# Kernel tuning notes

Measured on AMD Instinct MI355X. Metric: run time of the kernel, lower is better.

Reference implementation:

```python
import jax, jax.numpy as jnp
import numpy as np
from jax import lax

NPOINT = 1024
K = 32
GN_GROUPS = 32
EPS = 1e-5


def farthest_point_sample(xyz, npoint):
    # xyz: (B,N,3) -> idx (B,npoint). Deterministic start at index 0.
    B, N, _ = xyz.shape
    dist0 = jnp.full((B, N), 1e10, dtype=xyz.dtype)
    far0 = jnp.zeros((B,), dtype=jnp.int32)
    barange = jnp.arange(B)

    def step(carry, _):
        dist, far = carry
        centroid = xyz[barange, far][:, None, :]              # (B,1,3)
        d = jnp.sum((xyz - centroid) ** 2, axis=-1)           # (B,N)
        dist = jnp.minimum(dist, d)
        far_new = jnp.argmax(dist, axis=-1).astype(jnp.int32)
        return (dist, far_new), far

    _, idxs = lax.scan(step, (dist0, far0), None, length=npoint)
    return idxs.T  # (B,npoint)


def conv1x1(x, w, b):
    # x: (B,Cin,M,K), w: (Cout,Cin)
    return jnp.einsum('oc,bcmk->bomk', w, x) + b[None, :, None, None]


def group_norm(x, gamma, beta, groups):
    B, C, M, Kk = x.shape
    xg = x.reshape(B, groups, C // groups, M, Kk)
    mu = xg.mean(axis=(2, 3, 4), keepdims=True)
    var = xg.var(axis=(2, 3, 4), keepdims=True)
    xg = (xg - mu) * lax.rsqrt(var + EPS)
    x = xg.reshape(B, C, M, Kk)
    return x * gamma[None, :, None, None] + beta[None, :, None, None]


def setup_inputs() -> dict:
    key = jax.random.key(0)
    ks = jax.random.split(key, 4)
    B, N, Cin = 16, 8192, 64
    hid, out_ch, in_total = 64, 128, 3 + Cin
    return {
        'xyz': jax.random.normal(ks[0], (B, N, 3), jnp.float32),
        'feat': jax.random.normal(ks[1], (B, N, Cin), jnp.float32),
        'w1': jax.random.normal(ks[2], (hid, in_total), jnp.float32) * 0.1,
        'b1': jnp.zeros((hid,), jnp.float32),
        'g1w': jnp.ones((hid,), jnp.float32),
        'g1b': jnp.zeros((hid,), jnp.float32),
        'w2': jax.random.normal(ks[3], (out_ch, hid), jnp.float32) * 0.1,
        'b2': jnp.zeros((out_ch,), jnp.float32),
        'g2w': jnp.ones((out_ch,), jnp.float32),
        'g2b': jnp.zeros((out_ch,), jnp.float32),
    }


def reference(xyz, feat, w1, b1, g1w, g1b, w2, b2, g2w, g2b):
    B, N, _ = xyz.shape
    M = min(NPOINT, N)
    k = min(K, N)

    fps_idx = farthest_point_sample(lax.stop_gradient(xyz), M)   # (B,M) ints
    batch = jnp.arange(B)[:, None]
    centroids = xyz[batch, fps_idx]                              # (B,M,3)

    # kNN via squared distances (same ordering as cdist p=2)
    d2 = (jnp.sum(centroids ** 2, -1)[:, :, None]
          + jnp.sum(xyz ** 2, -1)[:, None, :]
          - 2.0 * jnp.einsum('bmd,bnd->bmn', centroids, xyz))    # (B,M,N)
    knn_idx = lax.top_k(-d2, k)[1]                               # (B,M,k)

    b3 = jnp.arange(B)[:, None, None]
    group_xyz = xyz[b3, knn_idx]                                 # (B,M,k,3)
    delta = group_xyz - centroids[:, :, None, :]
    gfeat = feat[b3, knn_idx]                                    # (B,M,k,Cin)
    gf = jnp.concatenate([delta, gfeat], axis=-1)                # (B,M,k,3+Cin)
    x = jnp.transpose(gf, (0, 3, 1, 2))                          # (B,C,M,k)

    x = jax.nn.relu(group_norm(conv1x1(x, w1, b1), g1w, g1b, GN_GROUPS))
    x = jax.nn.relu(group_norm(conv1x1(x, w2, b2), g2w, g2b, GN_GROUPS))
    out = jnp.max(x, axis=-1)                                    # (B,out_ch,M)
    new_feat = jnp.transpose(out, (0, 2, 1))                     # (B,M,out_ch)
    return (centroids, new_feat)
```

## Files before the change

kernel.cpp:

```cpp
#include <hip/hip_runtime.h>
#include <cstdint>

#define BB 16
#define NN 8192
#define MM 1024
#define KNN 32
#define CIN 64
#define HID 64
#define OCH 128

#define KNN_OFF   0u
#define SUM1_OFF  524288u
#define SUM2_OFF  526336u
#define W2B_OFF   536576u
#define W1B_OFF   540672u
#define Y1_OFF    543744u
#define PTS4_OFF  Y1_OFF
#define FEAT16_OFF (Y1_OFF + 16777216u)

typedef unsigned long long u64;
typedef float f32x4 __attribute__((ext_vector_type(4)));
typedef float f32x2 __attribute__((ext_vector_type(2)));
typedef short bf16x8 __attribute__((ext_vector_type(8)));

__device__ __forceinline__ unsigned short f2bf(float f) {
  union { float f; unsigned u; } v; v.f = f;
  unsigned r = v.u + 0x7FFFu + ((v.u >> 16) & 1u);
  return (unsigned short)(r >> 16);
}

__device__ __forceinline__ float bf2f(unsigned short u) {
  return __uint_as_float((unsigned)u << 16);
}

__device__ __forceinline__ u64 wave_max_u64(u64 v) {
  #define DPP_RND(ctrl, rm)                                                     \
  {                                                                             \
    int lo_ = __builtin_amdgcn_update_dpp(0, (int)(unsigned)(v & 0xFFFFFFFFull),\
                                          ctrl, rm, 0xf, true);                 \
    int hi_ = __builtin_amdgcn_update_dpp(0, (int)(unsigned)(v >> 32),          \
                                          ctrl, rm, 0xf, true);                 \
    u64 o_ = ((u64)(unsigned)hi_ << 32) | (unsigned)lo_;                        \
    v = o_ > v ? o_ : v;                                                        \
  }
  DPP_RND(0x111, 0xf)
  DPP_RND(0x112, 0xf)
  DPP_RND(0x114, 0xf)
  DPP_RND(0x118, 0xf)
  DPP_RND(0x142, 0xa)
  DPP_RND(0x143, 0xc)
  #undef DPP_RND
  return v;
}

__global__ __launch_bounds__(256) void fps_init_kernel(const float* __restrict__ xyz,
                                                       const float* __restrict__ feat,
                                                       const float* __restrict__ w1,
                                                       const float* __restrict__ w2,
                                                       float* __restrict__ ws,
                                                       float* __restrict__ cent) {
  #pragma clang fp contract(off)
  __shared__ float4 sp4[NN];
  __shared__ u64 slots[MM];
  __shared__ u64 wred[2][4];
  const int tid = threadIdx.x;

  if (blockIdx.x >= 16) {
    const int t0 = (blockIdx.x - 16) * 256 + tid;
    const int stride = 240 * 256;
    for (int t = t0; t < 12288; t += stride) ws[SUM1_OFF + t] = 0.0f;
    for (int t = t0; t < 4096; t += stride) {
      unsigned lo = f2bf(w2[2 * t]);
      unsigned hi = f2bf(w2[2 * t + 1]);
      ((unsigned*)(ws + W2B_OFF))[t] = lo | (hi << 16);
    }
    for (int t = t0; t < 6144; t += stride) {
      int n = t / 96, kk = t % 96;
      float val = 0.0f;
      if (kk < 3) val = w1[n * 67 + kk];
      else if (kk >= 4 && kk < 68) val = w1[n * 67 + kk - 1];
      ((unsigned short*)(ws + W1B_OFF))[t] = f2bf(val);
    }
    for (int t = t0; t < BB * NN; t += stride) {
      float x = xyz[(size_t)t * 3], y = xyz[(size_t)t * 3 + 1], z = xyz[(size_t)t * 3 + 2];
      ((float4*)(ws + PTS4_OFF))[t] = make_float4(x, y, z, (x * x + y * y) + z * z);
    }
    for (int t = t0; t < 4194304; t += stride) {
      float2 fv = *(const float2*)(feat + 2 * (size_t)t);
      unsigned lo = f2bf(fv.x), hi = f2bf(fv.y);
      ((unsigned*)(ws + FEAT16_OFF))[t] = lo | (hi << 16);
    }
    return;
  }

  const int b = blockIdx.x;
  const int w = tid >> 6;
  const float* xp = xyz + (size_t)b * NN * 3;
  f32x2 px[16], py[16], pz[16];
  float dist0[16], dist1[16];
  #pragma unroll
  for (int i = 0; i < 16; ++i) {
    int n0 = tid + (2 * i) * 256, n1 = tid + (2 * i + 1) * 256;
    float x0 = xp[n0 * 3], y0 = xp[n0 * 3 + 1], z0 = xp[n0 * 3 + 2];
    float x1 = xp[n1 * 3], y1 = xp[n1 * 3 + 1], z1 = xp[n1 * 3 + 2];
    px[i] = (f32x2){x0, x1}; py[i] = (f32x2){y0, y1}; pz[i] = (f32x2){z0, z1};
    sp4[n0] = make_float4(x0, y0, z0, 0.0f);
    sp4[n1] = make_float4(x1, y1, z1, 0.0f);
    dist0[i] = 1e10f; dist1[i] = 1e10f;
  }
  __syncthreads();
  int far = 0;
  for (int step = 0; step < MM; ++step) {
    float4 c4 = sp4[far];
    f32x2 cx = (f32x2){c4.x, c4.x}, cy = (f32x2){c4.y, c4.y}, cz = (f32x2){c4.z, c4.z};
    float best = -1.0f; int bi = 0;
    #pragma unroll
    for (int i = 0; i < 16; ++i) {
      f32x2 dx = px[i] - cx, dy = py[i] - cy, dz = pz[i] - cz;
      f32x2 d = (dx * dx + dy * dy) + dz * dz;
      float dm0 = fminf(dist0[i], d.x);
      float dm1 = fminf(dist1[i], d.y);
      dist0[i] = dm0; dist1[i] = dm1;
      if (dm0 > best) { best = dm0; bi = tid + (2 * i) * 256; }
      if (dm1 > best) { best = dm1; bi = tid + (2 * i + 1) * 256; }
    }
    u64 key = ((u64)__float_as_uint(best) << 32) | (unsigned)(8191 - bi);
    key = wave_max_u64(key);
    const int p = step & 1;
    if ((tid & 63) == 63) wred[p][w] = key;
    __syncthreads();
    u64 k0 = wred[p][0], k1 = wred[p][1], k2 = wred[p][2], k3 = wred[p][3];
    u64 m01 = k0 > k1 ? k0 : k1;
    u64 m23 = k2 > k3 ? k2 : k3;
    u64 bk = m01 > m23 ? m01 : m23;
    if (tid == 0) slots[step] = bk;
    far = 8191 - (int)(unsigned)(bk & 0xFFFFFFFFull);
  }
  __syncthreads();
  float* co = cent + (size_t)b * MM * 3;
  for (int s = tid; s < MM; s += 256) {
    int fs = (s == 0) ? 0 : (8191 - (int)(unsigned)(slots[s - 1] & 0xFFFFFFFFull));
    float4 c = sp4[fs];
    co[s * 3 + 0] = c.x; co[s * 3 + 1] = c.y; co[s * 3 + 2] = c.z;
  }
}

__global__ __launch_bounds__(512) void knn_conv1_kernel(const float4* __restrict__ pts4,
                                                        const float* __restrict__ xyz,
                                                        const unsigned short* __restrict__ feat16,
                                                        const float* __restrict__ cent,
                                                        const unsigned short* __restrict__ w1b,
                                                        const float* __restrict__ b1,
                                                        float* __restrict__ y1,
                                                        float* __restrict__ sums1) {
  #pragma clang fp contract(off)
  __shared__ __align__(16) char smem[65536];
  __shared__ float s1acc[64], q1acc[64];
  unsigned* blo = (unsigned*)smem;
  unsigned* bhi = (unsigned*)(smem + 32768);
  u64* marea = (u64*)smem;
  int* knn_lds = (int*)smem;
  unsigned short* gsm = (unsigned short*)(smem + 8192);
  const int tid = threadIdx.x;
  const int lane = tid & 63;
  const int w = tid >> 6;
  const int b = blockIdx.x >> 4;
  const int mc = blockIdx.x & 15;
  const int m = (mc << 6) + lane;

  if (tid < 64) { s1acc[tid] = 0.0f; q1acc[tid] = 0.0f; }

  const float* cp = cent + ((size_t)b * MM + m) * 3;
  float cx = cp[0], cy = cp[1], cz = cp[2];
  float cn2 = (cx * cx + cy * cy) + cz * cz;
  u64 key[32];
  {
    u64 initk = ((u64)(__float_as_uint(3e38f) ^ 0x80000000u) << 32) | 0xFFFFFFFFull;
    #pragma unroll
    for (int j = 0; j < 32; ++j) key[j] = initk;
  }
  float kthf = 3e38f;

  auto insert = [&](u64 cand) {
    bool cprev = false; u64 kprev = 0;
    #pragma unroll
    for (int j = 0; j < 32; ++j) {
      bool cj = cand < key[j];
      u64 cur = key[j];
      u64 nv = cj ? cand : cur;
      key[j] = cprev ? kprev : nv;
      cprev = cj; kprev = cur;
    }
    unsigned hb = (unsigned)(key[31] >> 32);
    unsigned ob = (hb & 0x80000000u) ? (hb ^ 0x80000000u) : ~hb;
    kthf = __uint_as_float(ob);
  };

  int cnt = 0;
  auto flush = [&]() {
    int mcx = cnt;
    #pragma unroll
    for (int off = 1; off < 64; off <<= 1) { int o = __shfl_xor(mcx, off); mcx = o > mcx ? o : mcx; }
    for (int i = 0; i < mcx; ++i) {
      u64 cand = ((u64)bhi[i * 512 + tid] << 32) | blo[i * 512 + tid];
      if (i < cnt && cand < key[31]) insert(cand);
    }
    cnt = 0;
  };

  const int nbase = __builtin_amdgcn_readfirstlane(w * 1024);
  const float4* pb = pts4 + (size_t)b * NN + nbase;
  for (int n0 = 0; n0 < 1024; n0 += 8) {
    #pragma unroll
    for (int j = 0; j < 8; ++j) {
      int n = n0 + j;
      float4 p = pb[n];
      float dot = fmaf(cz, p.z, fmaf(cy, p.y, cx * p.x));
      float d2 = (cn2 + p.w) - 2.0f * dot;
      if (d2 <= kthf) {
        unsigned db = __float_as_uint(d2);
        unsigned fk = db ^ (((int)db < 0) ? 0xFFFFFFFFu : 0x80000000u);
        blo[cnt * 512 + tid] = (unsigned)(nbase + n);
        bhi[cnt * 512 + tid] = fk;
        cnt++;
      }
    }
    if (__ballot(cnt >= 9)) flush();
  }
  flush();
  __syncthreads();

  auto publish = [&](int a) {
    u64* ap = marea + a * 2048;
    #pragma unroll
    for (int j = 0; j < 32; ++j) ap[j * 64 + lane] = key[j];
  };
  auto merge_from = [&](int a) {
    u64* ap = marea + a * 2048;
    for (int j = 0; j < 32; ++j) {
      u64 cand = ap[j * 64 + lane];
      if (cand < key[31]) insert(cand);
    }
  };
  if (w & 1) publish(w >> 1);
  __syncthreads();
  if (!(w & 1)) merge_from(w >> 1);
  __syncthreads();
  if (w == 2) publish(0);
  if (w == 6) publish(1);
  __syncthreads();
  if (w == 0) merge_from(0);
  if (w == 4) merge_from(1);
  __syncthreads();
  if (w == 4) publish(0);
  __syncthreads();
  if (w == 0) {
    merge_from(0);
    #pragma unroll
    for (int j = 0; j < 32; ++j)
      knn_lds[lane * 32 + j] = (int)(key[j] & 0xFFFFFFFFull);
  }
  __syncthreads();

  const int quad = lane >> 4, lr = lane & 15;
  unsigned short* gf = gsm + w * (32 * 104);

  {
    int row = lane >> 1, h = (lane & 1) * 16;
    ushort4 z4 = {0, 0, 0, 0};
    *(ushort4*)(gf + row * 104 + 64 + h + 0)  = z4;
    *(ushort4*)(gf + row * 104 + 64 + h + 4)  = z4;
    *(ushort4*)(gf + row * 104 + 64 + h + 8)  = z4;
    *(ushort4*)(gf + row * 104 + 64 + h + 12) = z4;
  }
  bf16x8 bw[4][3];
  float b1v[4];
  #pragma unroll
  for (int nt = 0; nt < 4; ++nt) {
    #pragma unroll
    for (int ks = 0; ks < 3; ++ks)
      bw[nt][ks] = *(const bf16x8*)(w1b + (size_t)(nt * 16 + lr) * 96 + ks * 32 + quad * 8);
    b1v[nt] = b1[nt * 16 + lr];
  }
  float s_nt[4] = {0.f, 0.f, 0.f, 0.f};
  float q_nt[4] = {0.f, 0.f, 0.f, 0.f};
  const unsigned short* fb = feat16 + (size_t)b * NN * 64;

  for (int r = 0; r < 8; ++r) {
    const int lm = w * 8 + r;
    const int wid = b * 1024 + (mc << 6) + lm;
    int idxv = 0;
    if (lane < 32) idxv = knn_lds[lm * 32 + lane];
    __builtin_amdgcn_s_waitcnt(0);
    __builtin_amdgcn_wave_barrier();
    const float* cq = cent + (size_t)wid * 3;
    float ccx = cq[0], ccy = cq[1], ccz = cq[2];
    if (lane < 32) {
      const float* pp = xyz + ((size_t)b * NN + idxv) * 3;
      ushort4 dv;
      dv.x = f2bf(pp[0] - ccx); dv.y = f2bf(pp[1] - ccy); dv.z = f2bf(pp[2] - ccz);
      dv.w = 0;
      *(ushort4*)(gf + lane * 104) = dv;
    }
    #pragma unroll
    for (int i = 0; i < 4; ++i) {
      int v = i * 64 + lane;
      int row = v >> 3, part = v & 7;
      int ridx = __shfl(idxv, row);
      uint4 fv = *(const uint4*)(fb + (size_t)ridx * 64 + part * 8);
      *(uint2*)(gf + row * 104 + 4 + part * 8)     = make_uint2(fv.x, fv.y);
      *(uint2*)(gf + row * 104 + 4 + part * 8 + 4) = make_uint2(fv.z, fv.w);
    }
    __builtin_amdgcn_s_waitcnt(0);
    __builtin_amdgcn_wave_barrier();

    f32x4 acc[2][4];
    #pragma unroll
    for (int mt = 0; mt < 2; ++mt)
      #pragma unroll
      for (int nt = 0; nt < 4; ++nt)
        acc[mt][nt] = (f32x4){0.f, 0.f, 0.f, 0.f};
    #pragma unroll
    for (int ks = 0; ks < 3; ++ks) {
      bf16x8 a0 = *(const bf16x8*)(gf + (0 + lr) * 104 + ks * 32 + quad * 8);
      bf16x8 a1 = *(const bf16x8*)(gf + (16 + lr) * 104 + ks * 32 + quad * 8);
      #pragma unroll
      for (int nt = 0; nt < 4; ++nt) {
        acc[0][nt] = __builtin_amdgcn_mfma_f32_16x16x32_bf16(a0, bw[nt][ks], acc[0][nt], 0, 0, 0);
        acc[1][nt] = __builtin_amdgcn_mfma_f32_16x16x32_bf16(a1, bw[nt][ks], acc[1][nt], 0, 0, 0);
      }
    }
    unsigned short* yo16 = (unsigned short*)(y1 + (size_t)wid * 1024);
    #pragma unroll
    for (int mt = 0; mt < 2; ++mt)
      #pragma unroll
      for (int rg = 0; rg < 4; ++rg) {
        int row = mt * 16 + quad * 4 + rg;
        #pragma unroll
        for (int nt = 0; nt < 4; ++nt) {
          float z = acc[mt][nt][rg] + b1v[nt];
          yo16[row * 64 + nt * 16 + lr] = f2bf(z);
          s_nt[nt] += z;
          q_nt[nt] = fmaf(z, z, q_nt[nt]);
        }
      }
  }
  #pragma unroll
  for (int nt = 0; nt < 4; ++nt) {
    float s = s_nt[nt], q = q_nt[nt];
    s += __shfl_xor(s, 16); s += __shfl_xor(s, 32);
    q += __shfl_xor(q, 16); q += __shfl_xor(q, 32);
    if (quad == 0) {
      atomicAdd(&s1acc[nt * 16 + lr], s);
      atomicAdd(&q1acc[nt * 16 + lr], q);
    }
  }
  __syncthreads();
  if (tid < 64) {
    atomicAdd(&sums1[b * 128 + tid], s1acc[tid]);
    atomicAdd(&sums1[b * 128 + 64 + tid], q1acc[tid]);
  }
}

struct Conv2Frag {
  bf16x8 bfr[8][2];
  float  b2v[8];
};

__device__ __forceinline__ void load_w2_frags(const unsigned short* __restrict__ w2b,
                                              const float* __restrict__ b2,
                                              int lane, Conv2Frag& F) {
  const int quad = lane >> 4, lr = lane & 15;
  #pragma unroll
  for (int nt = 0; nt < 8; ++nt) {
    #pragma unroll
    for (int t = 0; t < 2; ++t)
      F.bfr[nt][t] = *(const bf16x8*)(w2b + (size_t)(nt * 16 + lr) * 64 + t * 32 + quad * 8);
    F.b2v[nt] = b2[nt * 16 + lr];
  }
}

__device__ __forceinline__ void conv2_wave_mfma(const float* __restrict__ y1,
                                                const float* a1s,
                                                const float* d1s,
                                                unsigned short* __restrict__ hrow,
                                                int wid, int lane,
                                                const Conv2Frag& F,
                                                f32x4 acc[2][8]) {
  const int quad = lane >> 4, lr = lane & 15;
  const int r = lane >> 1, c0 = (lane & 1) * 32;
  const unsigned short* yrow16 =
      (const unsigned short*)(y1 + (size_t)wid * 1024) + r * 64 + c0;
  const float4* ap = (const float4*)(a1s + c0);
  const float4* dp = (const float4*)(d1s + c0);
  #pragma unroll
  for (int gg = 0; gg < 4; ++gg) {
    bf16x8 yv = *(const bf16x8*)(yrow16 + gg * 8);
    float4 av0 = ap[gg * 2],     dv0 = dp[gg * 2];
    float4 av1 = ap[gg * 2 + 1], dv1 = dp[gg * 2 + 1];
    ushort4 s0, s1;
    s0.x = f2bf(fmaxf(0.0f, fmaf(bf2f((unsigned short)yv[0]), av0.x, dv0.x)));
    s0.y = f2bf(fmaxf(0.0f, fmaf(bf2f((unsigned short)yv[1]), av0.y, dv0.y)));
    s0.z = f2bf(fmaxf(0.0f, fmaf(bf2f((unsigned short)yv[2]), av0.z, dv0.z)));
    s0.w = f2bf(fmaxf(0.0f, fmaf(bf2f((unsigned short)yv[3]), av0.w, dv0.w)));
    s1.x = f2bf(fmaxf(0.0f, fmaf(bf2f((unsigned short)yv[4]), av1.x, dv1.x)));
    s1.y = f2bf(fmaxf(0.0f, fmaf(bf2f((unsigned short)yv[5]), av1.y, dv1.y)));
    s1.z = f2bf(fmaxf(0.0f, fmaf(bf2f((unsigned short)yv[6]), av1.z, dv1.z)));
    s1.w = f2bf(fmaxf(0.0f, fmaf(bf2f((unsigned short)yv[7]), av1.w, dv1.w)));
    *(ushort4*)(hrow + r * 72 + c0 + 8 * gg)     = s0;
    *(ushort4*)(hrow + r * 72 + c0 + 8 * gg + 4) = s1;
  }
  __builtin_amdgcn_s_waitcnt(0);
  __builtin_amdgcn_wave_barrier();
  #pragma unroll
  for (int mt = 0; mt < 2; ++mt)
    #pragma unroll
    for (int nt = 0; nt < 8; ++nt)
      acc[mt][nt] = (f32x4){0.f, 0.f, 0.f, 0.f};
  #pragma unroll
  for (int t = 0; t < 2; ++t) {
    bf16x8 a0 = *(const bf16x8*)(hrow + (0 + lr) * 72 + t * 32 + quad * 8);
    bf16x8 a1f = *(const bf16x8*)(hrow + (16 + lr) * 72 + t * 32 + quad * 8);
    #pragma unroll
    for (int nt = 0; nt < 8; ++nt) {
      acc[0][nt] = __builtin_amdgcn_mfma_f32_16x16x32_bf16(a0,  F.bfr[nt][t], acc[0][nt], 0, 0, 0);
      acc[1][nt] = __builtin_amdgcn_mfma_f32_16x16x32_bf16(a1f, F.bfr[nt][t], acc[1][nt], 0, 0, 0);
    }
  }
}

__global__ __launch_bounds__(256) void conv2_stats_kernel(float* __restrict__ y1,
                                                          const float* __restrict__ sums1,
                                                          const float* __restrict__ g1w,
                                                          const float* __restrict__ g1b,
                                                          const unsigned short* __restrict__ w2b,
                                                          const float* __restrict__ b2,
                                                          float* __restrict__ sums2) {
  __shared__ __align__(16) unsigned short hsm[4][32 * 72];
  __shared__ float sacc[128], qacc[128];
  __shared__ float a1s[64], d1s[64];
  const int tid = threadIdx.x, lane = tid & 63, w = tid >> 6;
  const int wid = blockIdx.x * 4 + w;
  const int b = blockIdx.x >> 8;
  if (tid < 128) { sacc[tid] = 0.0f; qacc[tid] = 0.0f; }
  if (tid < 64) {
    int c = tid, g = c >> 1;
    float S = sums1[b * 128 + g * 2] + sums1[b * 128 + g * 2 + 1];
    float Q = sums1[b * 128 + 64 + g * 2] + sums1[b * 128 + 64 + g * 2 + 1];
    float mu = S * (1.0f / 65536.0f);
    float var = Q * (1.0f / 65536.0f) - mu * mu;
    float rs = 1.0f / sqrtf(var + 1e-5f);
    float ga = g1w[c];
    a1s[c] = rs * ga;
    d1s[c] = g1b[c] - mu * rs * ga;
  }
  __syncthreads();
  Conv2Frag F;
  load_w2_frags(w2b, b2, lane, F);
  f32x4 acc[2][8];
  conv2_wave_mfma(y1, a1s, d1s, hsm[w], wid, lane, F, acc);
  const int lr = lane & 15;
  float zmx[8], zmn[8];
  #pragma unroll
  for (int nt = 0; nt < 8; ++nt) {
    float s = 0, q = 0, mx = -3e38f, mn = 3e38f;
    #pragma unroll
    for (int mt = 0; mt < 2; ++mt)
      #pragma unroll
      for (int rg = 0; rg < 4; ++rg) {
        float z = acc[mt][nt][rg] + F.b2v[nt];
        s += z; q = fmaf(z, z, q);
        mx = fmaxf(mx, z); mn = fminf(mn, z);
      }
    atomicAdd(&sacc[nt * 16 + lr], s);
    atomicAdd(&qacc[nt * 16 + lr], q);
    mx = fmaxf(mx, __shfl_xor(mx, 16)); mx = fmaxf(mx, __shfl_xor(mx, 32));
    mn = fminf(mn, __shfl_xor(mn, 16)); mn = fminf(mn, __shfl_xor(mn, 32));
    zmx[nt] = mx; zmn[nt] = mn;
  }
  if (lane < 16) {
    float* zp = y1 + (size_t)wid * 1024;
    #pragma unroll
    for (int nt = 0; nt < 8; ++nt) {
      zp[nt * 16 + lr] = zmx[nt];
      zp[128 + nt * 16 + lr] = zmn[nt];
    }
  }
  __syncthreads();
  if (tid < 128) {
    atomicAdd(&sums2[b * 256 + tid], sacc[tid]);
    atomicAdd(&sums2[b * 256 + 128 + tid], qacc[tid]);
  }
}

__global__ __launch_bounds__(256) void final_lite(const float* __restrict__ y1,
                                                  const float* __restrict__ sums2,
                                                  const float* __restrict__ g2w,
                                                  const float* __restrict__ g2b,
                                                  float* __restrict__ nf) {
  __shared__ float a2s[128], d2s[128];
  const int tid = threadIdx.x;
  const int wid0 = blockIdx.x * 2;
  const int b = wid0 >> 10;
  if (tid < 128) {
    int c = tid, g = c >> 2;
    float S = ((sums2[b * 256 + g * 4] + sums2[b * 256 + g * 4 + 1])
               + sums2[b * 256 + g * 4 + 2]) + sums2[b * 256 + g * 4 + 3];
    float Q = ((sums2[b * 256 + 128 + g * 4] + sums2[b * 256 + 128 + g * 4 + 1])
               + sums2[b * 256 + 128 + g * 4 + 2]) + sums2[b * 256 + 128 + g * 4 + 3];
    float mu = S * (1.0f / 131072.0f);
    float var = Q * (1.0f / 131072.0f) - mu * mu;
    float rs = 1.0f / sqrtf(var + 1e-5f);
    float ga = g2w[c];
    a2s[c] = rs * ga;
    d2s[c] = g2b[c] - mu * rs * ga;
  }
  __syncthreads();
  int wid = wid0 + (tid >> 7), c = tid & 127;
  const float* zp = y1 + (size_t)wid * 1024;
  float zmx = zp[c];
  float zmn = zp[128 + c];
  float az = a2s[c], dz = d2s[c];
  float z = (az >= 0.0f) ? zmx : zmn;
  nf[(size_t)wid * 128 + c] = fmaxf(0.0f, fmaf(z, az, dz));
}

extern "C" void kernel_launch(void* const* d_in, const int* in_sizes, int n_in,
                              void* d_out, int out_size, void* d_ws, size_t ws_size,
                              hipStream_t stream) {
  const float* xyz  = (const float*)d_in[0];
  const float* feat = (const float*)d_in[1];
  const float* w1   = (const float*)d_in[2];
  const float* b1   = (const float*)d_in[3];
  const float* g1w  = (const float*)d_in[4];
  const float* g1b  = (const float*)d_in[5];
  const float* w2   = (const float*)d_in[6];
  const float* b2   = (const float*)d_in[7];
  const float* g2w  = (const float*)d_in[8];
  const float* g2b  = (const float*)d_in[9];
  float* ws = (float*)d_ws;
  float* cent = (float*)d_out;
  float* nf   = (float*)d_out + BB * MM * 3;
  const float4* pts4 = (const float4*)(ws + PTS4_OFF);
  float* sums1 = ws + SUM1_OFF;
  float* sums2 = ws + SUM2_OFF;
  const unsigned short* w2b = (const unsigned short*)(ws + W2B_OFF);
  const unsigned short* w1b = (const unsigned short*)(ws + W1B_OFF);
  const unsigned short* feat16 = (const unsigned short*)(ws + FEAT16_OFF);
  float* y1 = ws + Y1_OFF;

  hipLaunchKernelGGL(fps_init_kernel, dim3(256), dim3(256), 0, stream,
                     xyz, feat, w1, w2, ws, cent);
  hipLaunchKernelGGL(knn_conv1_kernel, dim3(256), dim3(512), 0, stream,
                     pts4, xyz, feat16, cent, w1b, b1, y1, sums1);
  hipLaunchKernelGGL(conv2_stats_kernel, dim3(4096), dim3(256), 0, stream,
                     y1, sums1, g1w, g1b, w2b, b2, sums2);
  hipLaunchKernelGGL(final_lite, dim3(8192), dim3(256), 0, stream,
                     y1, sums2, g2w, g2b, nf);
}
```

Measured before the change: 1.403 ms.

## Fuse kNN/conv1, conv2 stats and final epilogue into one kernel with per-batch barriers

The kNN+conv1, conv2+GroupNorm-stats and final normalize/max kernels are merged into one kernel launched with 256 blocks. Blocks of the same batch synchronize through global atomic counters with spin-waiting, so each GroupNorm's statistics are complete before the next stage reads them. Each wave now loops over 8 rows of conv2 and accumulates statistics in registers before a single shared-atomic reduction. This removes two kernel launches and their inter-kernel gaps. In exchange it relies on all blocks of a batch being resident at once, on the counters being zeroed beforehand, and it runs conv2 with far fewer waves than the old 4096-block launch.

```diff
diff --git a/kernel.cpp b/kernel.cpp
--- a/kernel.cpp
+++ b/kernel.cpp
@@ -9,9 +9,9 @@
 #define HID 64
 #define OCH 128
 
-#define KNN_OFF   0u
 #define SUM1_OFF  524288u
 #define SUM2_OFF  526336u
+#define CNT_OFF   530432u
 #define W2B_OFF   536576u
 #define W1B_OFF   540672u
 #define Y1_OFF    543744u
@@ -145,17 +145,96 @@
   }
 }
 
-__global__ __launch_bounds__(512) void knn_conv1_kernel(const float4* __restrict__ pts4,
-                                                        const float* __restrict__ xyz,
-                                                        const unsigned short* __restrict__ feat16,
-                                                        const float* __restrict__ cent,
-                                                        const unsigned short* __restrict__ w1b,
-                                                        const float* __restrict__ b1,
-                                                        float* __restrict__ y1,
-                                                        float* __restrict__ sums1) {
+struct Conv2Frag {
+  bf16x8 bfr[8][2];
+  float  b2v[8];
+};
+
+__device__ __forceinline__ void load_w2_frags(const unsigned short* __restrict__ w2b,
+                                              const float* __restrict__ b2,
+                                              int lane, Conv2Frag& F) {
+  const int quad = lane >> 4, lr = lane & 15;
+  #pragma unroll
+  for (int nt = 0; nt < 8; ++nt) {
+    #pragma unroll
+    for (int t = 0; t < 2; ++t)
+      F.bfr[nt][t] = *(const bf16x8*)(w2b + (size_t)(nt * 16 + lr) * 64 + t * 32 + quad * 8);
+    F.b2v[nt] = b2[nt * 16 + lr];
+  }
+}
+
+__device__ __forceinline__ void conv2_wave_mfma(const float* __restrict__ y1,
+                                                const float* a1s,
+                                                const float* d1s,
+                                                unsigned short* __restrict__ hrow,
+                                                int wid, int lane,
+                                                const Conv2Frag& F,
+                                                f32x4 acc[2][8]) {
+  const int quad = lane >> 4, lr = lane & 15;
+  const int r = lane >> 1, c0 = (lane & 1) * 32;
+  const unsigned short* yrow16 =
+      (const unsigned short*)(y1 + (size_t)wid * 1024) + r * 64 + c0;
+  const float4* ap = (const float4*)(a1s + c0);
+  const float4* dp = (const float4*)(d1s + c0);
+  #pragma unroll
+  for (int gg = 0; gg < 4; ++gg) {
+    bf16x8 yv = *(const bf16x8*)(yrow16 + gg * 8);
+    float4 av0 = ap[gg * 2],     dv0 = dp[gg * 2];
+    float4 av1 = ap[gg * 2 + 1], dv1 = dp[gg * 2 + 1];
+    ushort4 s0, s1;
+    s0.x = f2bf(fmaxf(0.0f, fmaf(bf2f((unsigned short)yv[0]), av0.x, dv0.x)));
+    s0.y = f2bf(fmaxf(0.0f, fmaf(bf2f((unsigned short)yv[1]), av0.y, dv0.y)));
+    s0.z = f2bf(fmaxf(0.0f, fmaf(bf2f((unsigned short)yv[2]), av0.z, dv0.z)));
+    s0.w = f2bf(fmaxf(0.0f, fmaf(bf2f((unsigned short)yv[3]), av0.w, dv0.w)));
+    s1.x = f2bf(fmaxf(0.0f, fmaf(bf2f((unsigned short)yv[4]), av1.x, dv1.x)));
+    s1.y = f2bf(fmaxf(0.0f, fmaf(bf2f((unsigned short)yv[5]), av1.y, dv1.y)));
+    s1.z = f2bf(fmaxf(0.0f, fmaf(bf2f((unsigned short)yv[6]), av1.z, dv1.z)));
+    s1.w = f2bf(fmaxf(0.0f, fmaf(bf2f((unsigned short)yv[7]), av1.w, dv1.w)));
+    *(ushort4*)(hrow + r * 72 + c0 + 8 * gg)     = s0;
+    *(ushort4*)(hrow + r * 72 + c0 + 8 * gg + 4) = s1;
+  }
+  __builtin_amdgcn_s_waitcnt(0);
+  __builtin_amdgcn_wave_barrier();
+  #pragma unroll
+  for (int mt = 0; mt < 2; ++mt)
+    #pragma unroll
+    for (int nt = 0; nt < 8; ++nt)
+      acc[mt][nt] = (f32x4){0.f, 0.f, 0.f, 0.f};
+  #pragma unroll
+  for (int t = 0; t < 2; ++t) {
+    bf16x8 a0 = *(const bf16x8*)(hrow + (0 + lr) * 72 + t * 32 + quad * 8);
+    bf16x8 a1f = *(const bf16x8*)(hrow + (16 + lr) * 72 + t * 32 + quad * 8);
+    #pragma unroll
+    for (int nt = 0; nt < 8; ++nt) {
+      acc[0][nt] = __builtin_amdgcn_mfma_f32_16x16x32_bf16(a0,  F.bfr[nt][t], acc[0][nt], 0, 0, 0);
+      acc[1][nt] = __builtin_amdgcn_mfma_f32_16x16x32_bf16(a1f, F.bfr[nt][t], acc[1][nt], 0, 0, 0);
+    }
+  }
+}
+
+__global__ __launch_bounds__(512) void mega_kernel(const float4* __restrict__ pts4,
+                                                   const float* __restrict__ xyz,
+                                                   const unsigned short* __restrict__ feat16,
+                                                   const float* __restrict__ cent,
+                                                   const unsigned short* __restrict__ w1b,
+                                                   const float* __restrict__ b1,
+                                                   const unsigned short* __restrict__ w2b,
+                                                   const float* __restrict__ b2,
+                                                   const float* __restrict__ g1w,
+                                                   const float* __restrict__ g1b,
+                                                   const float* __restrict__ g2w,
+                                                   const float* __restrict__ g2b,
+                                                   float* __restrict__ y1,
+                                                   float* __restrict__ sums1,
+                                                   float* __restrict__ sums2,
+                                                   int* __restrict__ cnt,
+                                                   float* __restrict__ nf) {
   #pragma clang fp contract(off)
   __shared__ __align__(16) char smem[65536];
   __shared__ float s1acc[64], q1acc[64];
+  __shared__ float sacc[128], qacc[128];
+  __shared__ float a1s[64], d1s[64];
+  __shared__ float a2s[128], d2s[128];
   unsigned* blo = (unsigned*)smem;
   unsigned* bhi = (unsigned*)(smem + 32768);
   u64* marea = (u64*)smem;
@@ -169,6 +248,7 @@
   const int m = (mc << 6) + lane;
 
   if (tid < 64) { s1acc[tid] = 0.0f; q1acc[tid] = 0.0f; }
+  if (tid < 128) { sacc[tid] = 0.0f; qacc[tid] = 0.0f; }
 
   const float* cp = cent + ((size_t)b * MM + m) * 3;
   float cx = cp[0], cy = cp[1], cz = cp[2];
@@ -196,16 +276,16 @@
     kthf = __uint_as_float(ob);
   };
 
-  int cnt = 0;
+  int cntl = 0;
   auto flush = [&]() {
-    int mcx = cnt;
+    int mcx = cntl;
     #pragma unroll
     for (int off = 1; off < 64; off <<= 1) { int o = __shfl_xor(mcx, off); mcx = o > mcx ? o : mcx; }
     for (int i = 0; i < mcx; ++i) {
       u64 cand = ((u64)bhi[i * 512 + tid] << 32) | blo[i * 512 + tid];
-      if (i < cnt && cand < key[31]) insert(cand);
-    }
-    cnt = 0;
+      if (i < cntl && cand < key[31]) insert(cand);
+    }
+    cntl = 0;
   };
 
   const int nbase = __builtin_amdgcn_readfirstlane(w * 1024);
@@ -220,12 +300,12 @@
       if (d2 <= kthf) {
         unsigned db = __float_as_uint(d2);
         unsigned fk = db ^ (((int)db < 0) ? 0xFFFFFFFFu : 0x80000000u);
-        blo[cnt * 512 + tid] = (unsigned)(nbase + n);
-        bhi[cnt * 512 + tid] = fk;
-        cnt++;
+        blo[cntl * 512 + tid] = (unsigned)(nbase + n);
+        bhi[cntl * 512 + tid] = fk;
+        cntl++;
       }
     }
-    if (__ballot(cnt >= 9)) flush();
+    if (__ballot(cntl >= 9)) flush();
   }
   flush();
   __syncthreads();
@@ -360,93 +440,24 @@
     atomicAdd(&sums1[b * 128 + tid], s1acc[tid]);
     atomicAdd(&sums1[b * 128 + 64 + tid], q1acc[tid]);
   }
-}
-
-struct Conv2Frag {
-  bf16x8 bfr[8][2];
-  float  b2v[8];
-};
-
-__device__ __forceinline__ void load_w2_frags(const unsigned short* __restrict__ w2b,
-                                              const float* __restrict__ b2,
-                                              int lane, Conv2Frag& F) {
-  const int quad = lane >> 4, lr = lane & 15;
-  #pragma unroll
-  for (int nt = 0; nt < 8; ++nt) {
-    #pragma unroll
-    for (int t = 0; t < 2; ++t)
-      F.bfr[nt][t] = *(const bf16x8*)(w2b + (size_t)(nt * 16 + lr) * 64 + t * 32 + quad * 8);
-    F.b2v[nt] = b2[nt * 16 + lr];
-  }
-}
-
-__device__ __forceinline__ void conv2_wave_mfma(const float* __restrict__ y1,
-                                                const float* a1s,
-                                                const float* d1s,
-                                                unsigned short* __restrict__ hrow,
-                                                int wid, int lane,
-                                                const Conv2Frag& F,
-                                                f32x4 acc[2][8]) {
-  const int quad = lane >> 4, lr = lane & 15;
-  const int r = lane >> 1, c0 = (lane & 1) * 32;
-  const unsigned short* yrow16 =
-      (const unsigned short*)(y1 + (size_t)wid * 1024) + r * 64 + c0;
-  const float4* ap = (const float4*)(a1s + c0);
-  const float4* dp = (const float4*)(d1s + c0);
-  #pragma unroll
-  for (int gg = 0; gg < 4; ++gg) {
-    bf16x8 yv = *(const bf16x8*)(yrow16 + gg * 8);
-    float4 av0 = ap[gg * 2],     dv0 = dp[gg * 2];
-    float4 av1 = ap[gg * 2 + 1], dv1 = dp[gg * 2 + 1];
-    ushort4 s0, s1;
-    s0.x = f2bf(fmaxf(0.0f, fmaf(bf2f((unsigned short)yv[0]), av0.x, dv0.x)));
-    s0.y = f2bf(fmaxf(0.0f, fmaf(bf2f((unsigned short)yv[1]), av0.y, dv0.y)));
-    s0.z = f2bf(fmaxf(0.0f, fmaf(bf2f((unsigned short)yv[2]), av0.z, dv0.z)));
-    s0.w = f2bf(fmaxf(0.0f, fmaf(bf2f((unsigned short)yv[3]), av0.w, dv0.w)));
-    s1.x = f2bf(fmaxf(0.0f, fmaf(bf2f((unsigned short)yv[4]), av1.x, dv1.x)));
-    s1.y = f2bf(fmaxf(0.0f, fmaf(bf2f((unsigned short)yv[5]), av1.y, dv1.y)));
-    s1.z = f2bf(fmaxf(0.0f, fmaf(bf2f((unsigned short)yv[6]), av1.z, dv1.z)));
-    s1.w = f2bf(fmaxf(0.0f, fmaf(bf2f((unsigned short)yv[7]), av1.w, dv1.w)));
-    *(ushort4*)(hrow + r * 72 + c0 + 8 * gg)     = s0;
-    *(ushort4*)(hrow + r * 72 + c0 + 8 * gg + 4) = s1;
-  }
-  __builtin_amdgcn_s_waitcnt(0);
-  __builtin_amdgcn_wave_barrier();
-  #pragma unroll
-  for (int mt = 0; mt < 2; ++mt)
-    #pragma unroll
-    for (int nt = 0; nt < 8; ++nt)
-      acc[mt][nt] = (f32x4){0.f, 0.f, 0.f, 0.f};
-  #pragma unroll
-  for (int t = 0; t < 2; ++t) {
-    bf16x8 a0 = *(const bf16x8*)(hrow + (0 + lr) * 72 + t * 32 + quad * 8);
-    bf16x8 a1f = *(const bf16x8*)(hrow + (16 + lr) * 72 + t * 32 + quad * 8);
-    #pragma unroll
-    for (int nt = 0; nt < 8; ++nt) {
-      acc[0][nt] = __builtin_amdgcn_mfma_f32_16x16x32_bf16(a0,  F.bfr[nt][t], acc[0][nt], 0, 0, 0);
-      acc[1][nt] = __builtin_amdgcn_mfma_f32_16x16x32_bf16(a1f, F.bfr[nt][t], acc[1][nt], 0, 0, 0);
-    }
-  }
-}
-
-__global__ __launch_bounds__(256) void conv2_stats_kernel(float* __restrict__ y1,
-                                                          const float* __restrict__ sums1,
-                                                          const float* __restrict__ g1w,
-                                                          const float* __restrict__ g1b,
-                                                          const unsigned short* __restrict__ w2b,
-                                                          const float* __restrict__ b2,
-                                                          float* __restrict__ sums2) {
-  __shared__ __align__(16) unsigned short hsm[4][32 * 72];
-  __shared__ float sacc[128], qacc[128];
-  __shared__ float a1s[64], d1s[64];
-  const int tid = threadIdx.x, lane = tid & 63, w = tid >> 6;
-  const int wid = blockIdx.x * 4 + w;
-  const int b = blockIdx.x >> 8;
-  if (tid < 128) { sacc[tid] = 0.0f; qacc[tid] = 0.0f; }
+  __syncthreads();
+
+  if (tid == 0) {
+    __threadfence();
+    __hip_atomic_fetch_add(&cnt[b], 1, __ATOMIC_RELEASE, __HIP_MEMORY_SCOPE_AGENT);
+    for (long it = 0; it < (1L << 30); ++it) {
+      if (__hip_atomic_load(&cnt[b], __ATOMIC_ACQUIRE, __HIP_MEMORY_SCOPE_AGENT) >= 16) break;
+      __builtin_amdgcn_s_sleep(2);
+    }
+  }
+  __syncthreads();
+
   if (tid < 64) {
     int c = tid, g = c >> 1;
-    float S = sums1[b * 128 + g * 2] + sums1[b * 128 + g * 2 + 1];
-    float Q = sums1[b * 128 + 64 + g * 2] + sums1[b * 128 + 64 + g * 2 + 1];
+    float S = __hip_atomic_load(&sums1[b * 128 + g * 2], __ATOMIC_RELAXED, __HIP_MEMORY_SCOPE_AGENT)
+            + __hip_atomic_load(&sums1[b * 128 + g * 2 + 1], __ATOMIC_RELAXED, __HIP_MEMORY_SCOPE_AGENT);
+    float Q = __hip_atomic_load(&sums1[b * 128 + 64 + g * 2], __ATOMIC_RELAXED, __HIP_MEMORY_SCOPE_AGENT)
+            + __hip_atomic_load(&sums1[b * 128 + 64 + g * 2 + 1], __ATOMIC_RELAXED, __HIP_MEMORY_SCOPE_AGENT);
     float mu = S * (1.0f / 65536.0f);
     float var = Q * (1.0f / 65536.0f) - mu * mu;
     float rs = 1.0f / sqrtf(var + 1e-5f);
@@ -455,35 +466,52 @@
     d1s[c] = g1b[c] - mu * rs * ga;
   }
   __syncthreads();
+
+  unsigned short* hrow = (unsigned short*)smem + w * 2304;
   Conv2Frag F;
   load_w2_frags(w2b, b2, lane, F);
-  f32x4 acc[2][8];
-  conv2_wave_mfma(y1, a1s, d1s, hsm[w], wid, lane, F, acc);
-  const int lr = lane & 15;
-  float zmx[8], zmn[8];
+  float s2_nt[8] = {0, 0, 0, 0, 0, 0, 0, 0};
+  float q2_nt[8] = {0, 0, 0, 0, 0, 0, 0, 0};
+  for (int r = 0; r < 8; ++r) {
+    const int wid = b * 1024 + (mc << 6) + w * 8 + r;
+    f32x4 acc[2][8];
+    conv2_wave_mfma(y1, a1s, d1s, hrow, wid, lane, F, acc);
+    float zmx[8], zmn[8];
+    #pragma unroll
+    for (int nt = 0; nt < 8; ++nt) {
+      float s = 0, q = 0, mx = -3e38f, mn = 3e38f;
+      #pragma unroll
+      for (int mt = 0; mt < 2; ++mt)
+        #pragma unroll
+        for (int rg = 0; rg < 4; ++rg) {
+          float z = acc[mt][nt][rg] + F.b2v[nt];
+          s += z; q = fmaf(z, z, q);
+          mx = fmaxf(mx, z); mn = fminf(mn, z);
+        }
+      s2_nt[nt] += s; q2_nt[nt] += q;
+      mx = fmaxf(mx, __shfl_xor(mx, 16)); mx = fmaxf(mx, __shfl_xor(mx, 32));
+      mn = fminf(mn, __shfl_xor(mn, 16)); mn = fminf(mn, __shfl_xor(mn, 32));
+      zmx[nt] = mx; zmn[nt] = mn;
+    }
+    if (lane < 16) {
+      float* zp = y1 + (size_t)wid * 1024;
+      #pragma unroll
+      for (int nt = 0; nt < 8; ++nt) {
+        zp[nt * 16 + lr] = zmx[nt];
+        zp[128 + nt * 16 + lr] = zmn[nt];
+      }
+    }
+    __builtin_amdgcn_s_waitcnt(0);
+    __builtin_amdgcn_wave_barrier();
+  }
   #pragma unroll
   for (int nt = 0; nt < 8; ++nt) {
-    float s = 0, q = 0, mx = -3e38f, mn = 3e38f;
-    #pragma unroll
-    for (int mt = 0; mt < 2; ++mt)
-      #pragma unroll
-      for (int rg = 0; rg < 4; ++rg) {
-        float z = acc[mt][nt][rg] + F.b2v[nt];
-        s += z; q = fmaf(z, z, q);
-        mx = fmaxf(mx, z); mn = fminf(mn, z);
-      }
-    atomicAdd(&sacc[nt * 16 + lr], s);
-    atomicAdd(&qacc[nt * 16 + lr], q);
-    mx = fmaxf(mx, __shfl_xor(mx, 16)); mx = fmaxf(mx, __shfl_xor(mx, 32));
-    mn = fminf(mn, __shfl_xor(mn, 16)); mn = fminf(mn, __shfl_xor(mn, 32));
-    zmx[nt] = mx; zmn[nt] = mn;
-  }
-  if (lane < 16) {
-    float* zp = y1 + (size_t)wid * 1024;
-    #pragma unroll
-    for (int nt = 0; nt < 8; ++nt) {
-      zp[nt * 16 + lr] = zmx[nt];
-      zp[128 + nt * 16 + lr] = zmn[nt];
+    float s = s2_nt[nt], q = q2_nt[nt];
+    s += __shfl_xor(s, 16); s += __shfl_xor(s, 32);
+    q += __shfl_xor(q, 16); q += __shfl_xor(q, 32);
+    if (quad == 0) {
+      atomicAdd(&sacc[nt * 16 + lr], s);
+      atomicAdd(&qacc[nt * 16 + lr], q);
     }
   }
   __syncthreads();
@@ -491,23 +519,30 @@
     atomicAdd(&sums2[b * 256 + tid], sacc[tid]);
     atomicAdd(&sums2[b * 256 + 128 + tid], qacc[tid]);
   }
-}
-
-__global__ __launch_bounds__(256) void final_lite(const float* __restrict__ y1,
-                                                  const float* __restrict__ sums2,
-                                                  const float* __restrict__ g2w,
-                                                  const float* __restrict__ g2b,
-                                                  float* __restrict__ nf) {
-  __shared__ float a2s[128], d2s[128];
-  const int tid = threadIdx.x;
-  const int wid0 = blockIdx.x * 2;
-  const int b = wid0 >> 10;
+  __syncthreads();
+
+  if (tid == 0) {
+    __threadfence();
+    __hip_atomic_fetch_add(&cnt[16 + b], 1, __ATOMIC_RELEASE, __HIP_MEMORY_SCOPE_AGENT);
+    for (long it = 0; it < (1L << 30); ++it) {
+      if (__hip_atomic_load(&cnt[16 + b], __ATOMIC_ACQUIRE, __HIP_MEMORY_SCOPE_AGENT) >= 16) break;
+      __builtin_amdgcn_s_sleep(2);
+    }
+  }
+  __syncthreads();
+
   if (tid < 128) {
     int c = tid, g = c >> 2;
-    float S = ((sums2[b * 256 + g * 4] + sums2[b * 256 + g * 4 + 1])
-               + sums2[b * 256 + g * 4 + 2]) + sums2[b * 256 + g * 4 + 3];
-    float Q = ((sums2[b * 256 + 128 + g * 4] + sums2[b * 256 + 128 + g * 4 + 1])
-               + sums2[b * 256 + 128 + g * 4 + 2]) + sums2[b * 256 + 128 + g * 4 + 3];
+    float s0 = __hip_atomic_load(&sums2[b * 256 + g * 4],     __ATOMIC_RELAXED, __HIP_MEMORY_SCOPE_AGENT);
+    float s1 = __hip_atomic_load(&sums2[b * 256 + g * 4 + 1], __ATOMIC_RELAXED, __HIP_MEMORY_SCOPE_AGENT);
+    float s2 = __hip_atomic_load(&sums2[b * 256 + g * 4 + 2], __ATOMIC_RELAXED, __HIP_MEMORY_SCOPE_AGENT);
+    float s3 = __hip_atomic_load(&sums2[b * 256 + g * 4 + 3], __ATOMIC_RELAXED, __HIP_MEMORY_SCOPE_AGENT);
+    float q0 = __hip_atomic_load(&sums2[b * 256 + 128 + g * 4],     __ATOMIC_RELAXED, __HIP_MEMORY_SCOPE_AGENT);
+    float q1 = __hip_atomic_load(&sums2[b * 256 + 128 + g * 4 + 1], __ATOMIC_RELAXED, __HIP_MEMORY_SCOPE_AGENT);
+    float q2 = __hip_atomic_load(&sums2[b * 256 + 128 + g * 4 + 2], __ATOMIC_RELAXED, __HIP_MEMORY_SCOPE_AGENT);
+    float q3 = __hip_atomic_load(&sums2[b * 256 + 128 + g * 4 + 3], __ATOMIC_RELAXED, __HIP_MEMORY_SCOPE_AGENT);
+    float S = ((s0 + s1) + s2) + s3;
+    float Q = ((q0 + q1) + q2) + q3;
     float mu = S * (1.0f / 131072.0f);
     float var = Q * (1.0f / 131072.0f) - mu * mu;
     float rs = 1.0f / sqrtf(var + 1e-5f);
@@ -516,13 +551,17 @@
     d2s[c] = g2b[c] - mu * rs * ga;
   }
   __syncthreads();
-  int wid = wid0 + (tid >> 7), c = tid & 127;
-  const float* zp = y1 + (size_t)wid * 1024;
-  float zmx = zp[c];
-  float zmn = zp[128 + c];
-  float az = a2s[c], dz = d2s[c];
-  float z = (az >= 0.0f) ? zmx : zmn;
-  nf[(size_t)wid * 128 + c] = fmaxf(0.0f, fmaf(z, az, dz));
+
+  for (int i = tid; i < 8192; i += 512) {
+    int lw = i >> 7, c = i & 127;
+    int wid = b * 1024 + (mc << 6) + lw;
+    const float* zp = y1 + (size_t)wid * 1024;
+    float zmx = zp[c];
+    float zmn = zp[128 + c];
+    float az = a2s[c], dz = d2s[c];
+    float z = (az >= 0.0f) ? zmx : zmn;
+    nf[(size_t)wid * 128 + c] = fmaxf(0.0f, fmaf(z, az, dz));
+  }
 }
 
 extern "C" void kernel_launch(void* const* d_in, const int* in_sizes, int n_in,
@@ -544,6 +583,7 @@
   const float4* pts4 = (const float4*)(ws + PTS4_OFF);
   float* sums1 = ws + SUM1_OFF;
   float* sums2 = ws + SUM2_OFF;
+  int*   cnt   = (int*)(ws + CNT_OFF);
   const unsigned short* w2b = (const unsigned short*)(ws + W2B_OFF);
   const unsigned short* w1b = (const unsigned short*)(ws + W1B_OFF);
   const unsigned short* feat16 = (const unsigned short*)(ws + FEAT16_OFF);
@@ -551,10 +591,7 @@
 
   hipLaunchKernelGGL(fps_init_kernel, dim3(256), dim3(256), 0, stream,
                      xyz, feat, w1, w2, ws, cent);
-  hipLaunchKernelGGL(knn_conv1_kernel, dim3(256), dim3(512), 0, stream,
-                     pts4, xyz, feat16, cent, w1b, b1, y1, sums1);
-  hipLaunchKernelGGL(conv2_stats_kernel, dim3(4096), dim3(256), 0, stream,
-                     y1, sums1, g1w, g1b, w2b, b2, sums2);
-  hipLaunchKernelGGL(final_lite, dim3(8192), dim3(256), 0, stream,
-                     y1, sums2, g2w, g2b, nf);
-}
+  hipLaunchKernelGGL(mega_kernel, dim3(256), dim3(512), 0, stream,
+                     pts4, xyz, feat16, cent, w1b, b1, w2b, b2,
+                     g1w, g1b, g2w, g2b, y1, sums1, sums2, cnt, nf);
+}
```

Result: faster. 1.372 ms (-2.2%).
